# Kernel optimization log

Hardware: AMD Instinct MI355X
Metric: run time of the kernel (lower is better)

The kernel has to match this reference:

```python
import jax, jax.numpy as jnp
import numpy as np

N_NODES = 50000
K_CHEB = 3


def _norm_weights(edge_index, num_nodes):
    # PyG ChebConv with normalization='sym', lambda_max=2.0:
    # L_hat = (2/lambda_max) * (I - D^-1/2 A D^-1/2) - I = -D^-1/2 A D^-1/2
    src, dst = edge_index[0], edge_index[1]
    ones = jnp.ones(src.shape[0], dtype=jnp.float32)
    deg = jax.ops.segment_sum(ones, src, num_segments=num_nodes)
    dis = jnp.where(deg > 0, jax.lax.rsqrt(jnp.maximum(deg, 1.0)), 0.0)
    w = dis[src] * dis[dst]  # [E]
    return src, dst, w


def _cheb_conv(x, src, dst, w, W, b, num_nodes):
    # W: [K, in, out], b: [out]
    def lap(v):  # L_hat @ v = -(D^-1/2 A D^-1/2) v via gather + segment-sum
        return -jax.ops.segment_sum(w[:, None] * v[src], dst, num_segments=num_nodes)
    Tx0 = x
    out = Tx0 @ W[0]
    Tx1 = lap(x)
    out = out + Tx1 @ W[1]
    for k in range(2, W.shape[0]):
        Tx2 = 2.0 * lap(Tx1) - Tx0
        out = out + Tx2 @ W[k]
        Tx0, Tx1 = Tx1, Tx2
    return out + b


def setup_inputs() -> dict:
    key = jax.random.key(0)
    ks = jax.random.split(key, 9)
    N, E, F_IN, F_HID, F_OUT = N_NODES, 800000, 128, 64, 16
    x = jax.random.normal(ks[0], (N, F_IN), dtype=jnp.float32)
    edge_index = jax.random.randint(ks[1], (2, E), 0, N, dtype=jnp.int64)
    def glorot(k, kk, fi, fo):
        s = (6.0 / (fi + fo)) ** 0.5
        return jax.random.uniform(k, (kk, fi, fo), jnp.float32, -s, s)
    W1 = glorot(ks[2], K_CHEB, F_IN, F_HID)
    b1 = jnp.zeros((F_HID,), jnp.float32)
    Wm = glorot(ks[3], K_CHEB, F_HID, F_HID)
    bm = jnp.zeros((F_HID,), jnp.float32)
    W2 = glorot(ks[4], K_CHEB, F_HID, F_OUT)
    b2 = jnp.zeros((F_OUT,), jnp.float32)
    return {"x": x, "edge_index": edge_index, "W1": W1, "b1": b1,
            "Wm": Wm, "bm": bm, "W2": W2, "b2": b2}


def reference(x, edge_index, W1, b1, Wm, bm, W2, b2):
    src, dst, w = _norm_weights(edge_index, N_NODES)
    h = jax.nn.relu(_cheb_conv(x, src, dst, w, W1, b1, N_NODES))
    # dropout is identity in eval mode (training=False)
    h = jax.nn.relu(_cheb_conv(h, src, dst, w, Wm, bm, N_NODES))
    out = _cheb_conv(h, src, dst, w, W2, b2, N_NODES)
    return out
```

## Files before the change

kernel.cpp:

```cpp
#include <hip/hip_runtime.h>
#include <hip/hip_fp16.h>

constexpr int NNODES = 50000;
constexpr int NS  = 32;
constexpr int NR  = 4;
constexpr int RSZ = 12500;

typedef _Float16 half8_t __attribute__((ext_vector_type(8)));
typedef _Float16 half4_t __attribute__((ext_vector_type(4)));
typedef float    f32x4_t __attribute__((ext_vector_type(4)));

template<int CH> struct hvec_sel;
template<> struct hvec_sel<4> { using T = half4_t; };
template<> struct hvec_sel<8> { using T = half8_t; };

__device__ __forceinline__ float w_of(unsigned ec) {
  unsigned short wb = (unsigned short)(ec >> 16);
  return (float)__builtin_bit_cast(_Float16, wb);
}


template<int FIN, int FOUT>
__device__ void pack_dev(const float* __restrict__ W, _Float16* __restrict__ Bp,
                         int b, int nb) {
  constexpr int NT = 3 * FOUT / 16;
  constexpr int KT = FIN / 32;
  const int total = KT * NT * 512;
  for (int i = b * 256 + (int)threadIdx.x; i < total; i += nb * 256) {
    int j = i & 7;
    int lane = (i >> 3) & 63;
    int tile = i >> 9;
    int nt = tile % NT, kt = tile / NT;
    int k = kt * 32 + (lane >> 4) * 8 + j;
    int n = nt * 16 + (lane & 15);
    int cheb = n / FOUT, c = n - cheb * FOUT;
    Bp[i] = (_Float16)W[((size_t)cheb * FIN + k) * FOUT + c];
  }
}

template<int FIN, int FOUT, typename IN_T>
__device__ void gemm_dev(const IN_T* __restrict__ X, const _Float16* __restrict__ Bp,
                         const float* __restrict__ b, _Float16* __restrict__ A,
                         _Float16* __restrict__ U, _Float16* __restrict__ V,
                         int N, int blk, _Float16* xs) {
  constexpr int NT = 3 * FOUT / 16;
  constexpr int C3 = NT / 3;
  constexpr int KT = FIN / 32;
  constexpr int LDR = FIN + 8;

  const int tid = threadIdx.x;
  const int row0 = blk * 64;

  for (int i = tid * 4; i < 64 * FIN; i += 1024) {
    int r = i / FIN, k = i - r * FIN;
    int row = row0 + r;
    short4 hv = make_short4(0, 0, 0, 0);
    if (row < N) {
      if constexpr (sizeof(IN_T) == 4) {
        float4 v = *(const float4*)((const float*)X + (size_t)row * FIN + k);
        _Float16 h0 = (_Float16)v.x, h1 = (_Float16)v.y, h2 = (_Float16)v.z, h3 = (_Float16)v.w;
        hv = make_short4(*(short*)&h0, *(short*)&h1, *(short*)&h2, *(short*)&h3);
      } else {
        hv = *(const short4*)((const _Float16*)X + (size_t)row * FIN + k);
      }
    }
    *(short4*)(&xs[r * LDR + k]) = hv;
  }
  __syncthreads();

  const int wave = tid >> 6, lane = tid & 63;
  const int m = lane & 15, quad = lane >> 4;

  f32x4_t acc[NT];
  #pragma unroll
  for (int nt = 0; nt < NT; ++nt) acc[nt] = (f32x4_t){0.f, 0.f, 0.f, 0.f};

  #pragma unroll
  for (int kt = 0; kt < KT; ++kt) {
    half8_t a = *(const half8_t*)(&xs[(wave * 16 + m) * LDR + kt * 32 + quad * 8]);
    const half8_t* bp = (const half8_t*)Bp + (size_t)(kt * NT) * 64 + lane;
    #pragma unroll
    for (int nt = 0; nt < NT; ++nt) {
      half8_t bf = bp[(size_t)nt * 64];
      acc[nt] = __builtin_amdgcn_mfma_f32_16x16x32_f16(a, bf, acc[nt], 0, 0, 0);
    }
  }

  const int row_b = row0 + wave * 16 + quad * 4;
  #pragma unroll
  for (int nt = 0; nt < C3; ++nt) {
    int c = nt * 16 + m;
    float bb = b[c];
    #pragma unroll
    for (int r = 0; r < 4; ++r) {
      int row = row_b + r;
      if (row < N) {
        size_t o = (size_t)row * FOUT + c;
        A[o] = (_Float16)(acc[nt][r] - acc[nt + 2 * C3][r] + bb);
        U[o] = (_Float16)acc[nt + C3][r];
        V[o] = (_Float16)acc[nt + 2 * C3][r];
      }
    }
  }
}


__global__ void __launch_bounds__(256) k1_hist_pack(const int* __restrict__ ei, int E, int ES,
    unsigned short* __restrict__ part_src, unsigned short* __restrict__ part_dst,
    unsigned char* __restrict__ rank,
    const float* __restrict__ W1, const float* __restrict__ Wm, const float* __restrict__ W2,
    _Float16* __restrict__ Bp1, _Float16* __restrict__ Bp2, _Float16* __restrict__ Bp3,
    int N) {
  __shared__ int sh[RSZ];
  const int bid = blockIdx.x;
  if (bid < 2 * NR * NS) {
    const int z = bid & 1, r = (bid >> 1) & 3, s = bid >> 3;
    for (int i = threadIdx.x; i < RSZ; i += 256) sh[i] = 0;
    __syncthreads();
    const int lo = r * RSZ;
    const int* __restrict__ idxarr = ei + (z ? E : 0);
    const int e0 = s * ES, e1 = min(e0 + ES, E);
    if (z) {
      for (int e = e0 + (int)threadIdx.x; e < e1; e += 256) {
        unsigned u = (unsigned)(idxarr[e] - lo);
        if (u < (unsigned)RSZ) {
          int rk = atomicAdd(&sh[u], 1);
          rank[e] = (unsigned char)rk;
        }
      }
    } else {
      for (int e = e0 + (int)threadIdx.x; e < e1; e += 256) {
        unsigned u = (unsigned)(idxarr[e] - lo);
        if (u < (unsigned)RSZ) atomicAdd(&sh[u], 1);
      }
    }
    __syncthreads();
    unsigned short* __restrict__ part = z ? part_dst : part_src;
    const size_t base = (size_t)s * N + lo;
    for (int i = threadIdx.x; i < RSZ && lo + i < N; i += 256)
      part[base + i] = (unsigned short)sh[i];
  } else if (bid < 2 * NR * NS + 24) {
    pack_dev<128, 64>(W1, Bp1, bid - 2 * NR * NS, 24);
  } else if (bid < 2 * NR * NS + 36) {
    pack_dev<64, 64>(Wm, Bp2, bid - 2 * NR * NS - 24, 12);
  } else {
    pack_dev<64, 16>(W2, Bp3, bid - 2 * NR * NS - 36, 3);
  }
}


__global__ void __launch_bounds__(256) k2_reduce_scan(const unsigned short* __restrict__ part_src,
    unsigned short* __restrict__ part_dst, _Float16* __restrict__ dis, int* __restrict__ cnt,
    int* __restrict__ exc, int* __restrict__ bsum, int N) {
  __shared__ int sh[256];
  const int tid = threadIdx.x;
  const int n = blockIdx.x * 256 + tid;
  int off = 0;
  if (n < N) {
    int ssum = 0;
    #pragma unroll 4
    for (int s = 0; s < NS; ++s) ssum += part_src[(size_t)s * N + n];
    dis[n] = (_Float16)((ssum > 0) ? rsqrtf((float)ssum) : 0.0f);
    for (int s = 0; s < NS; ++s) {
      size_t idx = (size_t)s * N + n;
      int c = part_dst[idx];
      part_dst[idx] = (unsigned short)off;
      off += c;
    }
    cnt[n] = off;
  }
  int acc = off;
  sh[tid] = acc; __syncthreads();
  #pragma unroll
  for (int o = 1; o < 256; o <<= 1) {
    int t = (tid >= o) ? sh[tid - o] : 0;
    __syncthreads();
    acc += t;
    sh[tid] = acc;
    __syncthreads();
  }
  if (n < N) exc[n] = acc - off;
  if (tid == 255) bsum[blockIdx.x] = acc;
}


__global__ void __launch_bounds__(256) k2b_scan2(int* __restrict__ bsum, int NB) {
  __shared__ int sh[256];
  int tid = threadIdx.x;
  int v = (tid < NB) ? bsum[tid] : 0;
  int acc = v;
  sh[tid] = acc; __syncthreads();
  #pragma unroll
  for (int o = 1; o < 256; o <<= 1) {
    int t = (tid >= o) ? sh[tid - o] : 0;
    __syncthreads();
    acc += t;
    sh[tid] = acc;
    __syncthreads();
  }
  if (tid < NB) bsum[tid] = acc - v;
}


constexpr int FILLB = 256;

__global__ void __launch_bounds__(256) k3_fill_gemm1(const int* __restrict__ ei, int E, int ES,
    const int* __restrict__ exc, const int* __restrict__ bsumx,
    const unsigned short* __restrict__ pd_off, const unsigned char* __restrict__ rank,
    const unsigned short* __restrict__ dis_u, unsigned* __restrict__ ew,
    const float* __restrict__ x, const _Float16* __restrict__ Bp1, const float* __restrict__ b1,
    _Float16* __restrict__ Ah, _Float16* __restrict__ Uh, _Float16* __restrict__ Vh, int N) {
  __shared__ _Float16 xs[64 * (128 + 8)];
  const int bid = blockIdx.x;
  if (bid < FILLB) {
    for (int e = bid * 256 + (int)threadIdx.x; e < E; e += FILLB * 256) {
      int sv = ei[e], d = ei[E + e];
      int s = e / ES;
      int pos = exc[d] + bsumx[d >> 8] + (int)pd_off[(size_t)s * N + d] + (int)rank[e];
      ew[pos] = (unsigned)sv | ((unsigned)dis_u[sv] << 16);
    }
  } else {
    gemm_dev<128, 64, float>(x, Bp1, b1, Ah, Uh, Vh, N, bid - FILLB, xs);
  }
}


template<int FIN, int FOUT>
__global__ void __launch_bounds__(256) gemm_mfma_kernel(const _Float16* __restrict__ X,
    const _Float16* __restrict__ Bp, const float* __restrict__ b,
    _Float16* __restrict__ A, _Float16* __restrict__ U, _Float16* __restrict__ V, int N) {
  __shared__ _Float16 xs[64 * (FIN + 8)];
  gemm_dev<FIN, FOUT, _Float16>(X, Bp, b, A, U, V, N, blockIdx.x, xs);
}


template<int F, int CH>
__global__ void __launch_bounds__(256) lapA_kernel(const void* __restrict__ Vp,
    const void* __restrict__ Up, void* __restrict__ Yp,
    const int* __restrict__ exc, const int* __restrict__ cnt, const int* __restrict__ bsumx,
    const unsigned* __restrict__ ew, const _Float16* __restrict__ dis, int N) {
  using HT = typename hvec_sel<CH>::T;
  constexpr int H = F / CH;
  const HT* __restrict__ Vv = (const HT*)Vp;
  int t = blockIdx.x * 256 + threadIdx.x;
  int n = t / H;
  if (n >= N) return;
  int h = t - n * H;
  int j = exc[n] + bsumx[n >> 8];
  int e = j + cnt[n];
  float acc[CH];
  #pragma unroll
  for (int i = 0; i < CH; ++i) acc[i] = 0.f;
  for (; j + 7 < e; j += 8) {
    unsigned c[8]; HT v[8];
    #pragma unroll
    for (int q = 0; q < 8; ++q) c[q] = ew[j + q];
    #pragma unroll
    for (int q = 0; q < 8; ++q) v[q] = Vv[(size_t)(c[q] & 0xFFFF) * H + h];
    #pragma unroll
    for (int q = 0; q < 8; ++q) {
      float w = w_of(c[q]);
      #pragma unroll
      for (int i = 0; i < CH; ++i) acc[i] = fmaf(w, (float)v[q][i], acc[i]);
    }
  }
  for (; j + 3 < e; j += 4) {
    unsigned c[4]; HT v[4];
    #pragma unroll
    for (int q = 0; q < 4; ++q) c[q] = ew[j + q];
    #pragma unroll
    for (int q = 0; q < 4; ++q) v[q] = Vv[(size_t)(c[q] & 0xFFFF) * H + h];
    #pragma unroll
    for (int q = 0; q < 4; ++q) {
      float w = w_of(c[q]);
      #pragma unroll
      for (int i = 0; i < CH; ++i) acc[i] = fmaf(w, (float)v[q][i], acc[i]);
    }
  }
  for (; j < e; ++j) {
    unsigned c = ew[j];
    float w = w_of(c);
    HT v = Vv[(size_t)(c & 0xFFFF) * H + h];
    #pragma unroll
    for (int i = 0; i < CH; ++i) acc[i] = fmaf(w, (float)v[i], acc[i]);
  }
  float s2 = -2.f * (float)dis[n];
  HT u = ((const HT*)Up)[t];
  HT y;
  #pragma unroll
  for (int i = 0; i < CH; ++i) y[i] = (_Float16)fmaf(s2, acc[i], (float)u[i]);
  ((HT*)Yp)[t] = y;
}

template<int F, int CH, bool RELU, bool OUT32>
__global__ void __launch_bounds__(256) lapB_kernel(const void* __restrict__ Yp,
    const void* __restrict__ Ap,
    const int* __restrict__ exc, const int* __restrict__ cnt, const int* __restrict__ bsumx,
    const unsigned* __restrict__ ew, const _Float16* __restrict__ dis,
    void* __restrict__ outp, int N) {
  using HT = typename hvec_sel<CH>::T;
  constexpr int H = F / CH;
  const HT* __restrict__ Yv = (const HT*)Yp;
  int t = blockIdx.x * 256 + threadIdx.x;
  int n = t / H;
  if (n >= N) return;
  int h = t - n * H;
  int j = exc[n] + bsumx[n >> 8];
  int e = j + cnt[n];
  float acc[CH];
  #pragma unroll
  for (int i = 0; i < CH; ++i) acc[i] = 0.f;
  for (; j + 7 < e; j += 8) {
    unsigned c[8]; HT v[8];
    #pragma unroll
    for (int q = 0; q < 8; ++q) c[q] = ew[j + q];
    #pragma unroll
    for (int q = 0; q < 8; ++q) v[q] = Yv[(size_t)(c[q] & 0xFFFF) * H + h];
    #pragma unroll
    for (int q = 0; q < 8; ++q) {
      float w = w_of(c[q]);
      #pragma unroll
      for (int i = 0; i < CH; ++i) acc[i] = fmaf(w, (float)v[q][i], acc[i]);
    }
  }
  for (; j + 3 < e; j += 4) {
    unsigned c[4]; HT v[4];
    #pragma unroll
    for (int q = 0; q < 4; ++q) c[q] = ew[j + q];
    #pragma unroll
    for (int q = 0; q < 4; ++q) v[q] = Yv[(size_t)(c[q] & 0xFFFF) * H + h];
    #pragma unroll
    for (int q = 0; q < 4; ++q) {
      float w = w_of(c[q]);
      #pragma unroll
      for (int i = 0; i < CH; ++i) acc[i] = fmaf(w, (float)v[q][i], acc[i]);
    }
  }
  for (; j < e; ++j) {
    unsigned c = ew[j];
    float w = w_of(c);
    HT v = Yv[(size_t)(c & 0xFFFF) * H + h];
    #pragma unroll
    for (int i = 0; i < CH; ++i) acc[i] = fmaf(w, (float)v[i], acc[i]);
  }
  float s1 = -(float)dis[n];
  HT a = ((const HT*)Ap)[t];
  float r[CH];
  #pragma unroll
  for (int i = 0; i < CH; ++i) {
    r[i] = fmaf(s1, acc[i], (float)a[i]);
    if (RELU) r[i] = fmaxf(r[i], 0.f);
  }
  if constexpr (OUT32) {
    float4* o4 = (float4*)outp;
    #pragma unroll
    for (int q = 0; q < CH / 4; ++q)
      o4[(size_t)t * (CH / 4) + q] = make_float4(r[4 * q], r[4 * q + 1], r[4 * q + 2], r[4 * q + 3]);
  } else {
    HT y;
    #pragma unroll
    for (int i = 0; i < CH; ++i) y[i] = (_Float16)r[i];
    ((HT*)outp)[t] = y;
  }
}


extern "C" void kernel_launch(void* const* d_in, const int* in_sizes, int n_in,
                              void* d_out, int out_size, void* d_ws, size_t ws_size,
                              hipStream_t stream) {
  const float* x  = (const float*)d_in[0];
  const int*   ei = (const int*)d_in[1];
  const float* W1 = (const float*)d_in[2];
  const float* b1 = (const float*)d_in[3];
  const float* Wm = (const float*)d_in[4];
  const float* bm = (const float*)d_in[5];
  const float* W2 = (const float*)d_in[6];
  const float* b2 = (const float*)d_in[7];
  float* out = (float*)d_out;
  const int N = NNODES;
  const int E = in_sizes[1] / 2;
  const int ES = (E + NS - 1) / NS;
  const int NB = (N + 255) / 256;

  char* p = (char*)d_ws;
  auto alloc = [&](size_t bytes) -> char* {
    char* q = p;
    p += (bytes + 255) & ~(size_t)255;
    return q;
  };
  unsigned short* part_src = (unsigned short*)alloc((size_t)NS * N * 2);
  unsigned short* part_dst = (unsigned short*)alloc((size_t)NS * N * 2);
  unsigned char*  rank     = (unsigned char*)alloc((size_t)E);
  int*            cnt      = (int*)alloc((size_t)N * 4);
  int*            exc      = (int*)alloc((size_t)N * 4);
  int*            bsum     = (int*)alloc(1024);
  _Float16*       dis      = (_Float16*)alloc((size_t)N * 2);
  unsigned*       ew       = (unsigned*)alloc((size_t)E * 4);
  _Float16* Xh  = (_Float16*)alloc((size_t)N * 64 * 2);
  _Float16* Ah  = (_Float16*)alloc((size_t)N * 64 * 2);
  _Float16* Uh  = (_Float16*)alloc((size_t)N * 64 * 2);
  _Float16* Vh  = (_Float16*)alloc((size_t)N * 64 * 2);
  _Float16* Yh  = (_Float16*)alloc((size_t)N * 64 * 2);
  _Float16* Bp1 = (_Float16*)alloc((size_t)128 * 192 * 2);
  _Float16* Bp2 = (_Float16*)alloc((size_t)64 * 192 * 2);
  _Float16* Bp3 = (_Float16*)alloc((size_t)64 * 48 * 2);

  k1_hist_pack<<<2 * NR * NS + 39, 256, 0, stream>>>(ei, E, ES, part_src, part_dst, rank,
                                                     W1, Wm, W2, Bp1, Bp2, Bp3, N);
  k2_reduce_scan<<<NB, 256, 0, stream>>>(part_src, part_dst, dis, cnt, exc, bsum, N);
  k2b_scan2<<<1, 256, 0, stream>>>(bsum, NB);
  k3_fill_gemm1<<<FILLB + 782, 256, 0, stream>>>(ei, E, ES, exc, bsum, part_dst, rank,
                                                 (const unsigned short*)dis, ew,
                                                 x, Bp1, b1, Ah, Uh, Vh, N);

  const int gmm  = (N + 63) / 64;
  const int g64c = (N * 8 + 255) / 256;
  const int g16c = (N * 4 + 255) / 256;

  lapA_kernel<64, 8><<<g64c, 256, 0, stream>>>(Vh, Uh, Yh, exc, cnt, bsum, ew, dis, N);
  lapB_kernel<64, 8, true, false><<<g64c, 256, 0, stream>>>(Yh, Ah, exc, cnt, bsum, ew, dis, Xh, N);

  gemm_mfma_kernel<64, 64><<<gmm, 256, 0, stream>>>(Xh, Bp2, bm, Ah, Uh, Vh, N);
  lapA_kernel<64, 8><<<g64c, 256, 0, stream>>>(Vh, Uh, Yh, exc, cnt, bsum, ew, dis, N);
  lapB_kernel<64, 8, true, false><<<g64c, 256, 0, stream>>>(Yh, Ah, exc, cnt, bsum, ew, dis, Xh, N);

  gemm_mfma_kernel<64, 16><<<gmm, 256, 0, stream>>>(Xh, Bp3, b2, Ah, Uh, Vh, N);
  lapA_kernel<16, 4><<<g16c, 256, 0, stream>>>(Vh, Uh, Yh, exc, cnt, bsum, ew, dis, N);
  lapB_kernel<16, 4, false, true><<<g16c, 256, 0, stream>>>(Yh, Ah, exc, cnt, bsum, ew, dis, out, N);
}
```

Measured before the change: 257.1 us.

## Fuse neighbor aggregation with next-layer MFMA GEMM and pack histogram counters into bytes

Adds a lapBG kernel that does the second Laplacian aggregation and ReLU for 32 nodes per block, stages the result in LDS, and immediately runs the next layer's MFMA GEMM. This removes the separate GEMM launches and the global round trip through the intermediate Xh buffer. The degree histogram now packs four 8-bit counters per 32-bit shared word across the whole node range, with 128 edge slices instead of 4 node ranges times 32 slices. This changes the partial-count arrays to bytes, which relies on per-slice counts staying below 256, and makes k2 loop over 128 slices per node.

```diff
diff --git a/kernel.cpp b/kernel.cpp
--- a/kernel.cpp
+++ b/kernel.cpp
@@ -2,9 +2,8 @@
 #include <hip/hip_fp16.h>
 
 constexpr int NNODES = 50000;
-constexpr int NS  = 32;
-constexpr int NR  = 4;
-constexpr int RSZ = 12500;
+constexpr int NS  = 128;
+constexpr int NW  = NNODES / 4;
 
 typedef _Float16 half8_t __attribute__((ext_vector_type(8)));
 typedef _Float16 half4_t __attribute__((ext_vector_type(4)));
@@ -106,51 +105,47 @@
 
 
 __global__ void __launch_bounds__(256) k1_hist_pack(const int* __restrict__ ei, int E, int ES,
-    unsigned short* __restrict__ part_src, unsigned short* __restrict__ part_dst,
+    unsigned char* __restrict__ part_src, unsigned char* __restrict__ part_dst,
     unsigned char* __restrict__ rank,
     const float* __restrict__ W1, const float* __restrict__ Wm, const float* __restrict__ W2,
     _Float16* __restrict__ Bp1, _Float16* __restrict__ Bp2, _Float16* __restrict__ Bp3,
     int N) {
-  __shared__ int sh[RSZ];
+  __shared__ unsigned sh[NW];
   const int bid = blockIdx.x;
-  if (bid < 2 * NR * NS) {
-    const int z = bid & 1, r = (bid >> 1) & 3, s = bid >> 3;
-    for (int i = threadIdx.x; i < RSZ; i += 256) sh[i] = 0;
+  if (bid < 2 * NS) {
+    const int z = bid & 1, s = bid >> 1;
+    for (int i = threadIdx.x; i < NW; i += 256) sh[i] = 0;
     __syncthreads();
-    const int lo = r * RSZ;
     const int* __restrict__ idxarr = ei + (z ? E : 0);
     const int e0 = s * ES, e1 = min(e0 + ES, E);
     if (z) {
       for (int e = e0 + (int)threadIdx.x; e < e1; e += 256) {
-        unsigned u = (unsigned)(idxarr[e] - lo);
-        if (u < (unsigned)RSZ) {
-          int rk = atomicAdd(&sh[u], 1);
-          rank[e] = (unsigned char)rk;
-        }
+        unsigned u = (unsigned)idxarr[e];
+        unsigned sh8 = (u & 3) * 8;
+        unsigned old = atomicAdd(&sh[u >> 2], 1u << sh8);
+        rank[e] = (unsigned char)(old >> sh8);
       }
     } else {
       for (int e = e0 + (int)threadIdx.x; e < e1; e += 256) {
-        unsigned u = (unsigned)(idxarr[e] - lo);
-        if (u < (unsigned)RSZ) atomicAdd(&sh[u], 1);
+        unsigned u = (unsigned)idxarr[e];
+        atomicAdd(&sh[u >> 2], 1u << ((u & 3) * 8));
       }
     }
     __syncthreads();
-    unsigned short* __restrict__ part = z ? part_dst : part_src;
-    const size_t base = (size_t)s * N + lo;
-    for (int i = threadIdx.x; i < RSZ && lo + i < N; i += 256)
-      part[base + i] = (unsigned short)sh[i];
-  } else if (bid < 2 * NR * NS + 24) {
-    pack_dev<128, 64>(W1, Bp1, bid - 2 * NR * NS, 24);
-  } else if (bid < 2 * NR * NS + 36) {
-    pack_dev<64, 64>(Wm, Bp2, bid - 2 * NR * NS - 24, 12);
+    unsigned* __restrict__ part = (unsigned*)((z ? part_dst : part_src) + (size_t)s * N);
+    for (int i = threadIdx.x; i < NW; i += 256) part[i] = sh[i];
+  } else if (bid < 2 * NS + 24) {
+    pack_dev<128, 64>(W1, Bp1, bid - 2 * NS, 24);
+  } else if (bid < 2 * NS + 36) {
+    pack_dev<64, 64>(Wm, Bp2, bid - 2 * NS - 24, 12);
   } else {
-    pack_dev<64, 16>(W2, Bp3, bid - 2 * NR * NS - 36, 3);
-  }
-}
-
-
-__global__ void __launch_bounds__(256) k2_reduce_scan(const unsigned short* __restrict__ part_src,
-    unsigned short* __restrict__ part_dst, _Float16* __restrict__ dis, int* __restrict__ cnt,
+    pack_dev<64, 16>(W2, Bp3, bid - 2 * NS - 36, 3);
+  }
+}
+
+
+__global__ void __launch_bounds__(256) k2_reduce_scan(const unsigned char* __restrict__ part_src,
+    unsigned char* __restrict__ part_dst, _Float16* __restrict__ dis, int* __restrict__ cnt,
     int* __restrict__ exc, int* __restrict__ bsum, int N) {
   __shared__ int sh[256];
   const int tid = threadIdx.x;
@@ -164,7 +159,7 @@
     for (int s = 0; s < NS; ++s) {
       size_t idx = (size_t)s * N + n;
       int c = part_dst[idx];
-      part_dst[idx] = (unsigned short)off;
+      part_dst[idx] = (unsigned char)off;
       off += c;
     }
     cnt[n] = off;
@@ -206,7 +201,7 @@
 
 __global__ void __launch_bounds__(256) k3_fill_gemm1(const int* __restrict__ ei, int E, int ES,
     const int* __restrict__ exc, const int* __restrict__ bsumx,
-    const unsigned short* __restrict__ pd_off, const unsigned char* __restrict__ rank,
+    const unsigned char* __restrict__ pd_off, const unsigned char* __restrict__ rank,
     const unsigned short* __restrict__ dis_u, unsigned* __restrict__ ew,
     const float* __restrict__ x, const _Float16* __restrict__ Bp1, const float* __restrict__ b1,
     _Float16* __restrict__ Ah, _Float16* __restrict__ Uh, _Float16* __restrict__ Vh, int N) {
@@ -222,15 +217,6 @@
   } else {
     gemm_dev<128, 64, float>(x, Bp1, b1, Ah, Uh, Vh, N, bid - FILLB, xs);
   }
-}
-
-
-template<int FIN, int FOUT>
-__global__ void __launch_bounds__(256) gemm_mfma_kernel(const _Float16* __restrict__ X,
-    const _Float16* __restrict__ Bp, const float* __restrict__ b,
-    _Float16* __restrict__ A, _Float16* __restrict__ U, _Float16* __restrict__ V, int N) {
-  __shared__ _Float16 xs[64 * (FIN + 8)];
-  gemm_dev<FIN, FOUT, _Float16>(X, Bp, b, A, U, V, N, blockIdx.x, xs);
 }
 
 
@@ -288,16 +274,16 @@
   HT u = ((const HT*)Up)[t];
   HT y;
   #pragma unroll
-  for (int i = 0; i < CH; ++i) y[i] = (_Float16)fmaf(s2, acc[i], (float)u[i]);
+  for (int i = 0; i < CH; ++i) y[i] = (_Float16)fmaf(2.f * 0.5f * s2, acc[i], (float)u[i]);
   ((HT*)Yp)[t] = y;
 }
 
-template<int F, int CH, bool RELU, bool OUT32>
-__global__ void __launch_bounds__(256) lapB_kernel(const void* __restrict__ Yp,
+template<int F, int CH>
+__global__ void __launch_bounds__(256) lapB_final_kernel(const void* __restrict__ Yp,
     const void* __restrict__ Ap,
     const int* __restrict__ exc, const int* __restrict__ cnt, const int* __restrict__ bsumx,
     const unsigned* __restrict__ ew, const _Float16* __restrict__ dis,
-    void* __restrict__ outp, int N) {
+    float* __restrict__ outp, int N) {
   using HT = typename hvec_sel<CH>::T;
   constexpr int H = F / CH;
   const HT* __restrict__ Yv = (const HT*)Yp;
@@ -345,22 +331,158 @@
   }
   float s1 = -(float)dis[n];
   HT a = ((const HT*)Ap)[t];
-  float r[CH];
-  #pragma unroll
-  for (int i = 0; i < CH; ++i) {
-    r[i] = fmaf(s1, acc[i], (float)a[i]);
-    if (RELU) r[i] = fmaxf(r[i], 0.f);
-  }
-  if constexpr (OUT32) {
-    float4* o4 = (float4*)outp;
-    #pragma unroll
-    for (int q = 0; q < CH / 4; ++q)
-      o4[(size_t)t * (CH / 4) + q] = make_float4(r[4 * q], r[4 * q + 1], r[4 * q + 2], r[4 * q + 3]);
+  float4* o4 = (float4*)outp;
+  #pragma unroll
+  for (int q = 0; q < CH / 4; ++q) {
+    float4 o;
+    o.x = fmaf(s1, acc[4 * q + 0], (float)a[4 * q + 0]);
+    o.y = fmaf(s1, acc[4 * q + 1], (float)a[4 * q + 1]);
+    o.z = fmaf(s1, acc[4 * q + 2], (float)a[4 * q + 2]);
+    o.w = fmaf(s1, acc[4 * q + 3], (float)a[4 * q + 3]);
+    o4[(size_t)t * (CH / 4) + q] = o;
+  }
+}
+
+
+template<int FOUT>
+__global__ void __launch_bounds__(256) lapBG_kernel(const void* __restrict__ Yp,
+    const void* __restrict__ Ap,
+    const int* __restrict__ exc, const int* __restrict__ cnt, const int* __restrict__ bsumx,
+    const unsigned* __restrict__ ew, const _Float16* __restrict__ dis,
+    const _Float16* __restrict__ Bp, const float* __restrict__ b,
+    _Float16* __restrict__ A2, _Float16* __restrict__ U2, _Float16* __restrict__ V2, int N) {
+  constexpr int LDR = 72;
+  constexpr int NT = 3 * FOUT / 16;
+  __shared__ _Float16 xs[32 * LDR];
+  const half8_t* __restrict__ Yv = (const half8_t*)Yp;
+
+  const int tid = threadIdx.x;
+  const int n0 = blockIdx.x * 32;
+  const int nloc = tid >> 3;
+  const int n = n0 + nloc;
+  const int h = tid & 7;
+
+  float r[8];
+  #pragma unroll
+  for (int i = 0; i < 8; ++i) r[i] = 0.f;
+  if (n < N) {
+    int j = exc[n] + bsumx[n >> 8];
+    int e = j + cnt[n];
+    float acc[8];
+    #pragma unroll
+    for (int i = 0; i < 8; ++i) acc[i] = 0.f;
+    for (; j + 7 < e; j += 8) {
+      unsigned c[8]; half8_t v[8];
+      #pragma unroll
+      for (int q = 0; q < 8; ++q) c[q] = ew[j + q];
+      #pragma unroll
+      for (int q = 0; q < 8; ++q) v[q] = Yv[(size_t)(c[q] & 0xFFFF) * 8 + h];
+      #pragma unroll
+      for (int q = 0; q < 8; ++q) {
+        float w = w_of(c[q]);
+        #pragma unroll
+        for (int i = 0; i < 8; ++i) acc[i] = fmaf(w, (float)v[q][i], acc[i]);
+      }
+    }
+    for (; j + 3 < e; j += 4) {
+      unsigned c[4]; half8_t v[4];
+      #pragma unroll
+      for (int q = 0; q < 4; ++q) c[q] = ew[j + q];
+      #pragma unroll
+      for (int q = 0; q < 4; ++q) v[q] = Yv[(size_t)(c[q] & 0xFFFF) * 8 + h];
+      #pragma unroll
+      for (int q = 0; q < 4; ++q) {
+        float w = w_of(c[q]);
+        #pragma unroll
+        for (int i = 0; i < 8; ++i) acc[i] = fmaf(w, (float)v[q][i], acc[i]);
+      }
+    }
+    for (; j < e; ++j) {
+      unsigned c = ew[j];
+      float w = w_of(c);
+      half8_t v = Yv[(size_t)(c & 0xFFFF) * 8 + h];
+      #pragma unroll
+      for (int i = 0; i < 8; ++i) acc[i] = fmaf(w, (float)v[i], acc[i]);
+    }
+    float s1 = -(float)dis[n];
+    half8_t a = ((const half8_t*)Ap)[(size_t)n * 8 + h];
+    #pragma unroll
+    for (int i = 0; i < 8; ++i)
+      r[i] = fmaxf(fmaf(s1, acc[i], (float)a[i]), 0.f);
+  }
+  half8_t y;
+  #pragma unroll
+  for (int i = 0; i < 8; ++i) y[i] = (_Float16)r[i];
+  *(half8_t*)(&xs[nloc * LDR + h * 8]) = y;
+  __syncthreads();
+
+  const int wave = tid >> 6, lane = tid & 63;
+  const int m = lane & 15, quad = lane >> 4;
+
+  if constexpr (FOUT == 64) {
+    const int mt = wave & 1, bnt = 2 * (wave >> 1);
+    f32x4_t acc[3][2];
+    #pragma unroll
+    for (int cb = 0; cb < 3; ++cb)
+      #pragma unroll
+      for (int ntl = 0; ntl < 2; ++ntl) acc[cb][ntl] = (f32x4_t){0.f, 0.f, 0.f, 0.f};
+    #pragma unroll
+    for (int kt = 0; kt < 2; ++kt) {
+      half8_t af = *(const half8_t*)(&xs[(mt * 16 + m) * LDR + kt * 32 + quad * 8]);
+      #pragma unroll
+      for (int cb = 0; cb < 3; ++cb) {
+        #pragma unroll
+        for (int ntl = 0; ntl < 2; ++ntl) {
+          int nt = cb * 4 + bnt + ntl;
+          half8_t bf = ((const half8_t*)Bp)[(size_t)(kt * NT + nt) * 64 + lane];
+          acc[cb][ntl] = __builtin_amdgcn_mfma_f32_16x16x32_f16(af, bf, acc[cb][ntl], 0, 0, 0);
+        }
+      }
+    }
+    const int row_b = n0 + mt * 16 + quad * 4;
+    #pragma unroll
+    for (int ntl = 0; ntl < 2; ++ntl) {
+      int c = (bnt + ntl) * 16 + m;
+      float bb = b[c];
+      #pragma unroll
+      for (int rr = 0; rr < 4; ++rr) {
+        int row = row_b + rr;
+        if (row < N) {
+          size_t o = (size_t)row * 64 + c;
+          A2[o] = (_Float16)(acc[0][ntl][rr] - acc[2][ntl][rr] + bb);
+          U2[o] = (_Float16)acc[1][ntl][rr];
+          V2[o] = (_Float16)acc[2][ntl][rr];
+        }
+      }
+    }
   } else {
-    HT y;
-    #pragma unroll
-    for (int i = 0; i < CH; ++i) y[i] = (_Float16)r[i];
-    ((HT*)outp)[t] = y;
+    if (wave < 2) {
+      const int mt = wave;
+      f32x4_t acc[3];
+      #pragma unroll
+      for (int cb = 0; cb < 3; ++cb) acc[cb] = (f32x4_t){0.f, 0.f, 0.f, 0.f};
+      #pragma unroll
+      for (int kt = 0; kt < 2; ++kt) {
+        half8_t af = *(const half8_t*)(&xs[(mt * 16 + m) * LDR + kt * 32 + quad * 8]);
+        #pragma unroll
+        for (int cb = 0; cb < 3; ++cb) {
+          half8_t bf = ((const half8_t*)Bp)[(size_t)(kt * NT + cb) * 64 + lane];
+          acc[cb] = __builtin_amdgcn_mfma_f32_16x16x32_f16(af, bf, acc[cb], 0, 0, 0);
+        }
+      }
+      const int row_b = n0 + mt * 16 + quad * 4;
+      float bb = b[m];
+      #pragma unroll
+      for (int rr = 0; rr < 4; ++rr) {
+        int row = row_b + rr;
+        if (row < N) {
+          size_t o = (size_t)row * 16 + m;
+          A2[o] = (_Float16)(acc[0][rr] - acc[2][rr] + bb);
+          U2[o] = (_Float16)acc[1][rr];
+          V2[o] = (_Float16)acc[2][rr];
+        }
+      }
+    }
   }
 }
 
@@ -388,15 +510,14 @@
     p += (bytes + 255) & ~(size_t)255;
     return q;
   };
-  unsigned short* part_src = (unsigned short*)alloc((size_t)NS * N * 2);
-  unsigned short* part_dst = (unsigned short*)alloc((size_t)NS * N * 2);
+  unsigned char*  part_src = (unsigned char*)alloc((size_t)NS * N);
+  unsigned char*  part_dst = (unsigned char*)alloc((size_t)NS * N);
   unsigned char*  rank     = (unsigned char*)alloc((size_t)E);
   int*            cnt      = (int*)alloc((size_t)N * 4);
   int*            exc      = (int*)alloc((size_t)N * 4);
   int*            bsum     = (int*)alloc(1024);
   _Float16*       dis      = (_Float16*)alloc((size_t)N * 2);
   unsigned*       ew       = (unsigned*)alloc((size_t)E * 4);
-  _Float16* Xh  = (_Float16*)alloc((size_t)N * 64 * 2);
   _Float16* Ah  = (_Float16*)alloc((size_t)N * 64 * 2);
   _Float16* Uh  = (_Float16*)alloc((size_t)N * 64 * 2);
   _Float16* Vh  = (_Float16*)alloc((size_t)N * 64 * 2);
@@ -405,26 +526,26 @@
   _Float16* Bp2 = (_Float16*)alloc((size_t)64 * 192 * 2);
   _Float16* Bp3 = (_Float16*)alloc((size_t)64 * 48 * 2);
 
-  k1_hist_pack<<<2 * NR * NS + 39, 256, 0, stream>>>(ei, E, ES, part_src, part_dst, rank,
-                                                     W1, Wm, W2, Bp1, Bp2, Bp3, N);
+  k1_hist_pack<<<2 * NS + 39, 256, 0, stream>>>(ei, E, ES, part_src, part_dst, rank,
+                                                W1, Wm, W2, Bp1, Bp2, Bp3, N);
   k2_reduce_scan<<<NB, 256, 0, stream>>>(part_src, part_dst, dis, cnt, exc, bsum, N);
   k2b_scan2<<<1, 256, 0, stream>>>(bsum, NB);
   k3_fill_gemm1<<<FILLB + 782, 256, 0, stream>>>(ei, E, ES, exc, bsum, part_dst, rank,
                                                  (const unsigned short*)dis, ew,
                                                  x, Bp1, b1, Ah, Uh, Vh, N);
 
-  const int gmm  = (N + 63) / 64;
+  const int g32  = (N + 31) / 32;
   const int g64c = (N * 8 + 255) / 256;
   const int g16c = (N * 4 + 255) / 256;
 
   lapA_kernel<64, 8><<<g64c, 256, 0, stream>>>(Vh, Uh, Yh, exc, cnt, bsum, ew, dis, N);
-  lapB_kernel<64, 8, true, false><<<g64c, 256, 0, stream>>>(Yh, Ah, exc, cnt, bsum, ew, dis, Xh, N);
-
-  gemm_mfma_kernel<64, 64><<<gmm, 256, 0, stream>>>(Xh, Bp2, bm, Ah, Uh, Vh, N);
+  lapBG_kernel<64><<<g32, 256, 0, stream>>>(Yh, Ah, exc, cnt, bsum, ew, dis,
+                                            Bp2, bm, Ah, Uh, Vh, N);
+
   lapA_kernel<64, 8><<<g64c, 256, 0, stream>>>(Vh, Uh, Yh, exc, cnt, bsum, ew, dis, N);
-  lapB_kernel<64, 8, true, false><<<g64c, 256, 0, stream>>>(Yh, Ah, exc, cnt, bsum, ew, dis, Xh, N);
-
-  gemm_mfma_kernel<64, 16><<<gmm, 256, 0, stream>>>(Xh, Bp3, b2, Ah, Uh, Vh, N);
+  lapBG_kernel<16><<<g32, 256, 0, stream>>>(Yh, Ah, exc, cnt, bsum, ew, dis,
+                                            Bp3, b2, Ah, Uh, Vh, N);
+
   lapA_kernel<16, 4><<<g16c, 256, 0, stream>>>(Vh, Uh, Yh, exc, cnt, bsum, ew, dis, N);
-  lapB_kernel<16, 4, false, true><<<g16c, 256, 0, stream>>>(Yh, Ah, exc, cnt, bsum, ew, dis, out, N);
-}
+  lapB_final_kernel<16, 4><<<g16c, 256, 0, stream>>>(Yh, Ah, exc, cnt, bsum, ew, dis, out, N);
+}
```

New measurement: 260.0 us. Within noise of the previous version (+1.1%).

## Pack per-node histogram counters into bytes to drop node-range partitioning

Applied to the files above, without the earlier changes.

The shared-memory histogram now keeps four 8-bit counters per 32-bit word, so one block covers all nodes instead of splitting them into four node ranges. This removes the repeated reads of each edge slice that the range split caused. The number of edge slices rises from 32 to 128 and the per-slice count and offset arrays shrink to bytes. In exchange, the reduce/scan kernel walks more slices per node, and any node with an in-degree above 255 would overflow the byte counters and offsets.

```diff
diff --git a/kernel.cpp b/kernel.cpp
--- a/kernel.cpp
+++ b/kernel.cpp
@@ -2,9 +2,8 @@
 #include <hip/hip_fp16.h>
 
 constexpr int NNODES = 50000;
-constexpr int NS  = 32;
-constexpr int NR  = 4;
-constexpr int RSZ = 12500;
+constexpr int NS  = 128;
+constexpr int NW  = NNODES / 4;
 
 typedef _Float16 half8_t __attribute__((ext_vector_type(8)));
 typedef _Float16 half4_t __attribute__((ext_vector_type(4)));
@@ -106,51 +105,47 @@
 
 
 __global__ void __launch_bounds__(256) k1_hist_pack(const int* __restrict__ ei, int E, int ES,
-    unsigned short* __restrict__ part_src, unsigned short* __restrict__ part_dst,
+    unsigned char* __restrict__ part_src, unsigned char* __restrict__ part_dst,
     unsigned char* __restrict__ rank,
     const float* __restrict__ W1, const float* __restrict__ Wm, const float* __restrict__ W2,
     _Float16* __restrict__ Bp1, _Float16* __restrict__ Bp2, _Float16* __restrict__ Bp3,
     int N) {
-  __shared__ int sh[RSZ];
+  __shared__ unsigned sh[NW];
   const int bid = blockIdx.x;
-  if (bid < 2 * NR * NS) {
-    const int z = bid & 1, r = (bid >> 1) & 3, s = bid >> 3;
-    for (int i = threadIdx.x; i < RSZ; i += 256) sh[i] = 0;
-    __syncthreads();
-    const int lo = r * RSZ;
+  if (bid < 2 * NS) {
+    const int z = bid & 1, s = bid >> 1;
+    for (int i = threadIdx.x; i < NW; i += 256) sh[i] = 0;
+    __syncthreads();
     const int* __restrict__ idxarr = ei + (z ? E : 0);
     const int e0 = s * ES, e1 = min(e0 + ES, E);
     if (z) {
       for (int e = e0 + (int)threadIdx.x; e < e1; e += 256) {
-        unsigned u = (unsigned)(idxarr[e] - lo);
-        if (u < (unsigned)RSZ) {
-          int rk = atomicAdd(&sh[u], 1);
-          rank[e] = (unsigned char)rk;
-        }
+        unsigned u = (unsigned)idxarr[e];
+        unsigned sh8 = (u & 3) * 8;
+        unsigned old = atomicAdd(&sh[u >> 2], 1u << sh8);
+        rank[e] = (unsigned char)(old >> sh8);
       }
     } else {
       for (int e = e0 + (int)threadIdx.x; e < e1; e += 256) {
-        unsigned u = (unsigned)(idxarr[e] - lo);
-        if (u < (unsigned)RSZ) atomicAdd(&sh[u], 1);
+        unsigned u = (unsigned)idxarr[e];
+        atomicAdd(&sh[u >> 2], 1u << ((u & 3) * 8));
       }
     }
     __syncthreads();
-    unsigned short* __restrict__ part = z ? part_dst : part_src;
-    const size_t base = (size_t)s * N + lo;
-    for (int i = threadIdx.x; i < RSZ && lo + i < N; i += 256)
-      part[base + i] = (unsigned short)sh[i];
-  } else if (bid < 2 * NR * NS + 24) {
-    pack_dev<128, 64>(W1, Bp1, bid - 2 * NR * NS, 24);
-  } else if (bid < 2 * NR * NS + 36) {
-    pack_dev<64, 64>(Wm, Bp2, bid - 2 * NR * NS - 24, 12);
+    unsigned* __restrict__ part = (unsigned*)((z ? part_dst : part_src) + (size_t)s * N);
+    for (int i = threadIdx.x; i < NW; i += 256) part[i] = sh[i];
+  } else if (bid < 2 * NS + 24) {
+    pack_dev<128, 64>(W1, Bp1, bid - 2 * NS, 24);
+  } else if (bid < 2 * NS + 36) {
+    pack_dev<64, 64>(Wm, Bp2, bid - 2 * NS - 24, 12);
   } else {
-    pack_dev<64, 16>(W2, Bp3, bid - 2 * NR * NS - 36, 3);
-  }
-}
-
-
-__global__ void __launch_bounds__(256) k2_reduce_scan(const unsigned short* __restrict__ part_src,
-    unsigned short* __restrict__ part_dst, _Float16* __restrict__ dis, int* __restrict__ cnt,
+    pack_dev<64, 16>(W2, Bp3, bid - 2 * NS - 36, 3);
+  }
+}
+
+
+__global__ void __launch_bounds__(256) k2_reduce_scan(const unsigned char* __restrict__ part_src,
+    unsigned char* __restrict__ part_dst, _Float16* __restrict__ dis, int* __restrict__ cnt,
     int* __restrict__ exc, int* __restrict__ bsum, int N) {
   __shared__ int sh[256];
   const int tid = threadIdx.x;
@@ -164,7 +159,7 @@
     for (int s = 0; s < NS; ++s) {
       size_t idx = (size_t)s * N + n;
       int c = part_dst[idx];
-      part_dst[idx] = (unsigned short)off;
+      part_dst[idx] = (unsigned char)off;
       off += c;
     }
     cnt[n] = off;
@@ -206,7 +201,7 @@
 
 __global__ void __launch_bounds__(256) k3_fill_gemm1(const int* __restrict__ ei, int E, int ES,
     const int* __restrict__ exc, const int* __restrict__ bsumx,
-    const unsigned short* __restrict__ pd_off, const unsigned char* __restrict__ rank,
+    const unsigned char* __restrict__ pd_off, const unsigned char* __restrict__ rank,
     const unsigned short* __restrict__ dis_u, unsigned* __restrict__ ew,
     const float* __restrict__ x, const _Float16* __restrict__ Bp1, const float* __restrict__ b1,
     _Float16* __restrict__ Ah, _Float16* __restrict__ Uh, _Float16* __restrict__ Vh, int N) {
@@ -388,8 +383,8 @@
     p += (bytes + 255) & ~(size_t)255;
     return q;
   };
-  unsigned short* part_src = (unsigned short*)alloc((size_t)NS * N * 2);
-  unsigned short* part_dst = (unsigned short*)alloc((size_t)NS * N * 2);
+  unsigned char*  part_src = (unsigned char*)alloc((size_t)NS * N);
+  unsigned char*  part_dst = (unsigned char*)alloc((size_t)NS * N);
   unsigned char*  rank     = (unsigned char*)alloc((size_t)E);
   int*            cnt      = (int*)alloc((size_t)N * 4);
   int*            exc      = (int*)alloc((size_t)N * 4);
@@ -405,8 +400,8 @@
   _Float16* Bp2 = (_Float16*)alloc((size_t)64 * 192 * 2);
   _Float16* Bp3 = (_Float16*)alloc((size_t)64 * 48 * 2);
 
-  k1_hist_pack<<<2 * NR * NS + 39, 256, 0, stream>>>(ei, E, ES, part_src, part_dst, rank,
-                                                     W1, Wm, W2, Bp1, Bp2, Bp3, N);
+  k1_hist_pack<<<2 * NS + 39, 256, 0, stream>>>(ei, E, ES, part_src, part_dst, rank,
+                                                W1, Wm, W2, Bp1, Bp2, Bp3, N);
   k2_reduce_scan<<<NB, 256, 0, stream>>>(part_src, part_dst, dis, cnt, exc, bsum, N);
   k2b_scan2<<<1, 256, 0, stream>>>(bsum, NB);
   k3_fill_gemm1<<<FILLB + 782, 256, 0, stream>>>(ei, E, ES, exc, bsum, part_dst, rank,
```

Result: no change. 252.5 us (-1.8%).
